# Kernel optimization log

Hardware: AMD Instinct MI355X
Metric: run time of the kernel (lower is better)

Reference implementation:

```python
import jax, jax.numpy as jnp
import numpy as np

RELEASE_PROB = 0.9
N = 16777216  # input_size: number of synapses


def setup_inputs() -> dict:
    key = jax.random.key(0)
    k1, k2, k3, k4, k5 = jax.random.split(key, 5)
    x = jax.random.normal(k1, (N,), dtype=jnp.float32)
    weights = jax.random.normal(k2, (N,), dtype=jnp.float32) * 0.1
    fatigue = jax.random.uniform(k3, (N,), dtype=jnp.float32)  # per-synapse fatigue state in (0,1]
    u = jax.random.uniform(k4, (N,), dtype=jnp.float32)        # per-synapse uniform draws for release
    threshold = jnp.abs(jax.random.normal(k5, (1,), dtype=jnp.float32) * 0.01)
    return {"x": x, "weights": weights, "fatigue": fatigue, "u": u, "threshold": threshold}


def reference(x, weights, fatigue, u, threshold):
    # Stochastic release: synapse transmits iff u < release_probability.
    mask = (u < RELEASE_PROB).astype(x.dtype)
    # weight * fatigue * input per synapse, masked, then summed.
    total = jnp.sum(mask * weights * fatigue * x)
    # Dynamic threshold: fire with tanh, else output 0.
    out = jnp.where(total > threshold[0], jnp.tanh(total), jnp.zeros((), dtype=x.dtype))
    return out
```

## Files before the change

### kernel.cpp

```cpp
#include <hip/hip_runtime.h>
#include <math.h>

#define BLOCK 256
#define GRID 2048
#define RELEASE_PROB 0.9f

__global__ __launch_bounds__(BLOCK) void neuron_partial(
    const float4* __restrict__ x,
    const float4* __restrict__ w,
    const float4* __restrict__ f,
    const float4* __restrict__ u,
    float* __restrict__ partials,
    int n4)
{
    const int tid = blockIdx.x * BLOCK + threadIdx.x;
    const int stride = GRID * BLOCK;

    float acc = 0.0f;
    for (int i = tid; i < n4; i += stride) {
        const float4 xv = x[i];
        const float4 wv = w[i];
        const float4 fv = f[i];
        const float4 uv = u[i];
        acc += (uv.x < RELEASE_PROB) ? wv.x * fv.x * xv.x : 0.0f;
        acc += (uv.y < RELEASE_PROB) ? wv.y * fv.y * xv.y : 0.0f;
        acc += (uv.z < RELEASE_PROB) ? wv.z * fv.z * xv.z : 0.0f;
        acc += (uv.w < RELEASE_PROB) ? wv.w * fv.w * xv.w : 0.0f;
    }

    #pragma unroll
    for (int off = 32; off > 0; off >>= 1)
        acc += __shfl_down(acc, off, 64);

    __shared__ float sm[BLOCK / 64];
    const int lane = threadIdx.x & 63;
    const int wave = threadIdx.x >> 6;
    if (lane == 0) sm[wave] = acc;
    __syncthreads();

    if (threadIdx.x == 0) {
        float s = 0.0f;
        #pragma unroll
        for (int i = 0; i < BLOCK / 64; ++i) s += sm[i];
        partials[blockIdx.x] = s;
    }
}

__global__ __launch_bounds__(BLOCK) void neuron_final(
    const float* __restrict__ partials,
    const float* __restrict__ threshold,
    float* __restrict__ out)
{
    float acc = 0.0f;
    for (int i = threadIdx.x; i < GRID; i += BLOCK)
        acc += partials[i];

    #pragma unroll
    for (int off = 32; off > 0; off >>= 1)
        acc += __shfl_down(acc, off, 64);

    __shared__ float sm[BLOCK / 64];
    const int lane = threadIdx.x & 63;
    const int wave = threadIdx.x >> 6;
    if (lane == 0) sm[wave] = acc;
    __syncthreads();

    if (threadIdx.x == 0) {
        float total = 0.0f;
        #pragma unroll
        for (int i = 0; i < BLOCK / 64; ++i) total += sm[i];
        out[0] = (total > threshold[0]) ? tanhf(total) : 0.0f;
    }
}

extern "C" void kernel_launch(void* const* d_in, const int* in_sizes, int n_in,
                              void* d_out, int out_size, void* d_ws, size_t ws_size,
                              hipStream_t stream)
{
    const float* x   = (const float*)d_in[0];
    const float* w   = (const float*)d_in[1];
    const float* f   = (const float*)d_in[2];
    const float* u   = (const float*)d_in[3];
    const float* thr = (const float*)d_in[4];

    float* out = (float*)d_out;
    float* partials = (float*)d_ws;

    const int n  = in_sizes[0];
    const int n4 = n / 4;

    neuron_partial<<<GRID, BLOCK, 0, stream>>>(
        (const float4*)x, (const float4*)w, (const float4*)f, (const float4*)u,
        partials, n4);

    neuron_final<<<1, BLOCK, 0, stream>>>(partials, thr, out);
}
```

Before: 46.09 us.

## Fuse final reduction via last-block atomic counter and unroll load loop by two

```diff
diff --git a/kernel.cpp b/kernel.cpp
--- a/kernel.cpp
+++ b/kernel.cpp
@@ -5,23 +5,37 @@
 #define GRID 2048
 #define RELEASE_PROB 0.9f
 
-__global__ __launch_bounds__(BLOCK) void neuron_partial(
+__global__ __launch_bounds__(BLOCK) void neuron_fused(
     const float4* __restrict__ x,
     const float4* __restrict__ w,
     const float4* __restrict__ f,
     const float4* __restrict__ u,
+    const float* __restrict__ threshold,
+    float* __restrict__ out,
     float* __restrict__ partials,
+    unsigned int* __restrict__ counter,
     int n4)
 {
     const int tid = blockIdx.x * BLOCK + threadIdx.x;
     const int stride = GRID * BLOCK;
 
     float acc = 0.0f;
-    for (int i = tid; i < n4; i += stride) {
-        const float4 xv = x[i];
-        const float4 wv = w[i];
-        const float4 fv = f[i];
-        const float4 uv = u[i];
+    int i = tid;
+    for (; i + stride < n4; i += 2 * stride) {
+        const int j = i + stride;
+        const float4 xv0 = x[i], wv0 = w[i], fv0 = f[i], uv0 = u[i];
+        const float4 xv1 = x[j], wv1 = w[j], fv1 = f[j], uv1 = u[j];
+        acc += (uv0.x < RELEASE_PROB) ? wv0.x * fv0.x * xv0.x : 0.0f;
+        acc += (uv0.y < RELEASE_PROB) ? wv0.y * fv0.y * xv0.y : 0.0f;
+        acc += (uv0.z < RELEASE_PROB) ? wv0.z * fv0.z * xv0.z : 0.0f;
+        acc += (uv0.w < RELEASE_PROB) ? wv0.w * fv0.w * xv0.w : 0.0f;
+        acc += (uv1.x < RELEASE_PROB) ? wv1.x * fv1.x * xv1.x : 0.0f;
+        acc += (uv1.y < RELEASE_PROB) ? wv1.y * fv1.y * xv1.y : 0.0f;
+        acc += (uv1.z < RELEASE_PROB) ? wv1.z * fv1.z * xv1.z : 0.0f;
+        acc += (uv1.w < RELEASE_PROB) ? wv1.w * fv1.w * xv1.w : 0.0f;
+    }
+    for (; i < n4; i += stride) {
+        const float4 xv = x[i], wv = w[i], fv = f[i], uv = u[i];
         acc += (uv.x < RELEASE_PROB) ? wv.x * fv.x * xv.x : 0.0f;
         acc += (uv.y < RELEASE_PROB) ? wv.y * fv.y * xv.y : 0.0f;
         acc += (uv.z < RELEASE_PROB) ? wv.z * fv.z * xv.z : 0.0f;
@@ -33,6 +47,7 @@
         acc += __shfl_down(acc, off, 64);
 
     __shared__ float sm[BLOCK / 64];
+    __shared__ int is_last;
     const int lane = threadIdx.x & 63;
     const int wave = threadIdx.x >> 6;
     if (lane == 0) sm[wave] = acc;
@@ -41,35 +56,31 @@
     if (threadIdx.x == 0) {
         float s = 0.0f;
         #pragma unroll
-        for (int i = 0; i < BLOCK / 64; ++i) s += sm[i];
-        partials[blockIdx.x] = s;
+        for (int k = 0; k < BLOCK / 64; ++k) s += sm[k];
+        __hip_atomic_store(&partials[blockIdx.x], s,
+                           __ATOMIC_RELEASE, __HIP_MEMORY_SCOPE_AGENT);
+        const unsigned int t = __hip_atomic_fetch_add(
+            counter, 1u, __ATOMIC_ACQ_REL, __HIP_MEMORY_SCOPE_AGENT);
+        is_last = (t == GRID - 1) ? 1 : 0;
     }
-}
-
-__global__ __launch_bounds__(BLOCK) void neuron_final(
-    const float* __restrict__ partials,
-    const float* __restrict__ threshold,
-    float* __restrict__ out)
-{
-    float acc = 0.0f;
-    for (int i = threadIdx.x; i < GRID; i += BLOCK)
-        acc += partials[i];
-
-    #pragma unroll
-    for (int off = 32; off > 0; off >>= 1)
-        acc += __shfl_down(acc, off, 64);
-
-    __shared__ float sm[BLOCK / 64];
-    const int lane = threadIdx.x & 63;
-    const int wave = threadIdx.x >> 6;
-    if (lane == 0) sm[wave] = acc;
     __syncthreads();
 
-    if (threadIdx.x == 0) {
-        float total = 0.0f;
+    if (is_last) {
+        float acc2 = 0.0f;
+        for (int k = threadIdx.x; k < GRID; k += BLOCK)
+            acc2 += __hip_atomic_load(&partials[k],
+                                      __ATOMIC_RELAXED, __HIP_MEMORY_SCOPE_AGENT);
         #pragma unroll
-        for (int i = 0; i < BLOCK / 64; ++i) total += sm[i];
-        out[0] = (total > threshold[0]) ? tanhf(total) : 0.0f;
+        for (int off = 32; off > 0; off >>= 1)
+            acc2 += __shfl_down(acc2, off, 64);
+        if (lane == 0) sm[wave] = acc2;
+        __syncthreads();
+        if (threadIdx.x == 0) {
+            float total = 0.0f;
+            #pragma unroll
+            for (int k = 0; k < BLOCK / 64; ++k) total += sm[k];
+            out[0] = (total > threshold[0]) ? tanhf(total) : 0.0f;
+        }
     }
 }
 
@@ -85,13 +96,14 @@
 
     float* out = (float*)d_out;
     float* partials = (float*)d_ws;
+    unsigned int* counter = (unsigned int*)((char*)d_ws + GRID * sizeof(float));
 
     const int n  = in_sizes[0];
     const int n4 = n / 4;
 
-    neuron_partial<<<GRID, BLOCK, 0, stream>>>(
+    hipMemsetAsync(counter, 0, sizeof(unsigned int), stream);
+
+    neuron_fused<<<GRID, BLOCK, 0, stream>>>(
         (const float4*)x, (const float4*)w, (const float4*)f, (const float4*)u,
-        partials, n4);
-
-    neuron_final<<<1, BLOCK, 0, stream>>>(partials, thr, out);
+        thr, out, partials, counter, n4);
 }
```

After: 168.7 us. 3.66x slower.
